# Performance work log

Hardware: AMD Instinct MI355X
Metric: run time of the kernel (lower is better)

The kernel has to match this reference:

```python
import jax, jax.numpy as jnp
import numpy as np

B, T, D, H = 4096, 256, 64, 256


def _uniform(key, shape, bound):
    return jax.random.uniform(key, shape, jnp.float32, -bound, bound)


def setup_inputs() -> dict:
    key = jax.random.key(0)
    ks = jax.random.split(key, 12)
    bnd = 1.0 / np.sqrt(H)
    return {
        "x": jax.random.normal(ks[0], (B, T, D), jnp.float32),
        "h_1": jnp.zeros((B, H), jnp.float32),
        "h_2": jnp.zeros((B, H), jnp.float32),
        # GRUCell 1: input D -> hidden H (PyTorch layout: [3H, in])
        "W_ih1": _uniform(ks[1], (3 * H, D), bnd),
        "W_hh1": _uniform(ks[2], (3 * H, H), bnd),
        "b_ih1": _uniform(ks[3], (3 * H,), bnd),
        "b_hh1": _uniform(ks[4], (3 * H,), bnd),
        # GRUCell 2: input H -> hidden H
        "W_ih2": _uniform(ks[5], (3 * H, H), bnd),
        "W_hh2": _uniform(ks[6], (3 * H, H), bnd),
        "b_ih2": _uniform(ks[7], (3 * H,), bnd),
        "b_hh2": _uniform(ks[8], (3 * H,), bnd),
        # Linear head H -> D
        "W_fc": _uniform(ks[9], (D, H), bnd),
        "b_fc": _uniform(ks[10], (D,), bnd),
    }


def gru_cell(x, h, W_ih, W_hh, b_ih, b_hh):
    # PyTorch GRUCell math: r,z,n gates stacked along first axis of W.
    gi = x @ W_ih.T + b_ih            # [B, 3H]
    gh = h @ W_hh.T + b_hh            # [B, 3H]
    i_r, i_z, i_n = jnp.split(gi, 3, axis=-1)
    h_r, h_z, h_n = jnp.split(gh, 3, axis=-1)
    r = jax.nn.sigmoid(i_r + h_r)
    z = jax.nn.sigmoid(i_z + h_z)
    n = jnp.tanh(i_n + r * h_n)
    return (1.0 - z) * n + z * h


def reference(x, h_1, h_2, W_ih1, W_hh1, b_ih1, b_hh1,
              W_ih2, W_hh2, b_ih2, b_hh2, W_fc, b_fc):
    xs = jnp.swapaxes(x, 0, 1)  # [T, B, D] for scan over time

    def step(carry, x_t):
        h1, h2 = carry
        h1 = gru_cell(x_t, h1, W_ih1, W_hh1, b_ih1, b_hh1)
        h2 = gru_cell(h1, h2, W_ih2, W_hh2, b_ih2, b_hh2)
        y_t = h2 @ W_fc.T + b_fc  # [B, D]
        return (h1, h2), y_t

    (h_1, h_2), ys = jax.lax.scan(step, (h_1, h_2), xs)
    output_seq = jnp.swapaxes(ys, 0, 1)  # [B, T, D]
    return output_seq, h_1, h_2
```

## Files before the change

### kernel.cpp

```cpp
#include <hip/hip_runtime.h>

#define Bn 4096
#define Tn 256
#define Dn 64
#define Hn 256

#define BT  32
#define NTH 512
#define NWG 128
#define LDH 264
#define LDX 72

typedef __attribute__((ext_vector_type(4))) float f32x4;
typedef __attribute__((ext_vector_type(8))) short bf16x8;
typedef __attribute__((ext_vector_type(4))) short s16x4;

#define MFMA16(a,b,c) __builtin_amdgcn_mfma_f32_16x16x32_bf16((a),(b),(c),0,0,0)

#define OFF_WIH1 0
#define OFF_WHH1 49152
#define OFF_WIH2 245760
#define OFF_WHH2 442368
#define OFF_WFC  638976
#define W_TOTAL  655360

__device__ __forceinline__ short f2b(float f){
  union { float fv; unsigned u; } v; v.fv = f;
  unsigned r = v.u + 0x7fffu + ((v.u >> 16) & 1u);
  return (short)(r >> 16);
}
__device__ __forceinline__ float sigm(float x){ return 1.f/(1.f+__expf(-x)); }
__device__ __forceinline__ float tanh_s(float x){ float e=__expf(2.f*x); return 1.f - 2.f/(e+1.f); }

__global__ void prep_weights(const float* __restrict__ Wih1, const float* __restrict__ Whh1,
                             const float* __restrict__ Wih2, const float* __restrict__ Whh2,
                             const float* __restrict__ Wfc, short* __restrict__ wsb){
  for (int i = blockIdx.x*blockDim.x + threadIdx.x; i < W_TOTAL; i += gridDim.x*blockDim.x){
    float v;
    if (i < OFF_WHH1)      v = Wih1[i - OFF_WIH1];
    else if (i < OFF_WIH2) v = Whh1[i - OFF_WHH1];
    else if (i < OFF_WHH2) v = Wih2[i - OFF_WIH2];
    else if (i < OFF_WFC)  v = Whh2[i - OFF_WHH2];
    else                   v = Wfc [i - OFF_WFC];
    wsb[i] = f2b(v);
  }
}

__global__ __launch_bounds__(NTH, 2) void gru_fused(
    const float* __restrict__ x,
    const float* __restrict__ h1_in, const float* __restrict__ h2_in,
    const float* __restrict__ b_ih1, const float* __restrict__ b_hh1,
    const float* __restrict__ b_ih2, const float* __restrict__ b_hh2,
    const float* __restrict__ b_fc,
    const short* __restrict__ wsb,
    float* __restrict__ out)
{
  __shared__ short h1b[BT*LDH];
  __shared__ short h2b[BT*LDH];
  __shared__ short xb [BT*LDX];

  const int tid = (int)threadIdx.x;
  const int w   = tid >> 6;
  const int l   = tid & 63;
  const int q   = l >> 4;
  const int r16 = l & 15;
  const int b0  = (int)blockIdx.x * BT;

  const short* Wih1 = wsb + OFF_WIH1;
  const short* Whh1 = wsb + OFF_WHH1;
  const short* Wih2 = wsb + OFF_WIH2;
  const short* Whh2 = wsb + OFF_WHH2;
  const short* Wfc  = wsb + OFF_WFC;

  float bi1[2][3], bh1v[2][3], bi2[2][3], bh2v[2][3];
#pragma unroll
  for (int c=0;c<2;++c)
#pragma unroll
    for (int g=0;g<3;++g){
      const int col = g*Hn + (2*w+c)*16 + r16;
      bi1 [c][g] = b_ih1[col];  bh1v[c][g] = b_hh1[col];
      bi2 [c][g] = b_ih2[col];  bh2v[c][g] = b_hh2[col];
    }
  const float bfc = b_fc[(w&3)*16 + r16];

  float h1s[2][2][4], h2s[2][2][4];
#pragma unroll
  for (int rt=0;rt<2;++rt)
#pragma unroll
    for (int c=0;c<2;++c)
#pragma unroll
      for (int j=0;j<4;++j){
        const int row = rt*16 + q*4 + j;
        const int col = (2*w+c)*16 + r16;
        const float v1 = h1_in[(size_t)(b0+row)*Hn + col];
        const float v2 = h2_in[(size_t)(b0+row)*Hn + col];
        h1s[rt][c][j] = v1;  h2s[rt][c][j] = v2;
        h1b[row*LDH + col] = f2b(v1);
        h2b[row*LDH + col] = f2b(v2);
      }
  __syncthreads();

  const int xr = tid >> 4;
  const int xd = (tid & 15) * 4;
  const f32x4 z4 = {0.f,0.f,0.f,0.f};

  for (int t=0; t<Tn; ++t){
    {
      const float4 xv = *(const float4*)(x + ((size_t)(b0+xr)*Tn + t)*Dn + xd);
      s16x4 pk; pk.x=f2b(xv.x); pk.y=f2b(xv.y); pk.z=f2b(xv.z); pk.w=f2b(xv.w);
      *(s16x4*)&xb[xr*LDX + xd] = pk;
    }
    __syncthreads();

    f32x4 gi[2][2][3], gh[2][2][3];
#pragma unroll
    for (int rt=0;rt<2;++rt)
#pragma unroll
      for (int c=0;c<2;++c)
#pragma unroll
        for (int g=0;g<3;++g){ gi[rt][c][g]=z4; gh[rt][c][g]=z4; }

#pragma unroll
    for (int k=0;k<2;++k){
      const bf16x8 ax0 = *(const bf16x8*)&xb[(r16   )*LDX + k*32 + q*8];
      const bf16x8 ax1 = *(const bf16x8*)&xb[(16+r16)*LDX + k*32 + q*8];
#pragma unroll
      for (int c=0;c<2;++c)
#pragma unroll
        for (int g=0;g<3;++g){
          const int col = g*Hn + (2*w+c)*16;
          const bf16x8 bx = *(const bf16x8*)&Wih1[(size_t)(col + r16)*Dn + k*32 + q*8];
          gi[0][c][g] = MFMA16(ax0, bx, gi[0][c][g]);
          gi[1][c][g] = MFMA16(ax1, bx, gi[1][c][g]);
        }
    }
    for (int k=0;k<8;++k){
      const bf16x8 a0 = *(const bf16x8*)&h1b[(r16   )*LDH + k*32 + q*8];
      const bf16x8 a1 = *(const bf16x8*)&h1b[(16+r16)*LDH + k*32 + q*8];
#pragma unroll
      for (int c=0;c<2;++c)
#pragma unroll
        for (int g=0;g<3;++g){
          const int col = g*Hn + (2*w+c)*16;
          const bf16x8 bb = *(const bf16x8*)&Whh1[(size_t)(col + r16)*Hn + k*32 + q*8];
          gh[0][c][g] = MFMA16(a0, bb, gh[0][c][g]);
          gh[1][c][g] = MFMA16(a1, bb, gh[1][c][g]);
        }
    }
    __syncthreads();

#pragma unroll
    for (int rt=0;rt<2;++rt)
#pragma unroll
      for (int c=0;c<2;++c){
        const int colb = (2*w+c)*16 + r16;
#pragma unroll
        for (int j=0;j<4;++j){
          const float rr = sigm(gi[rt][c][0][j]+bi1[c][0] + gh[rt][c][0][j]+bh1v[c][0]);
          const float zz = sigm(gi[rt][c][1][j]+bi1[c][1] + gh[rt][c][1][j]+bh1v[c][1]);
          const float nn = tanh_s(gi[rt][c][2][j]+bi1[c][2] + rr*(gh[rt][c][2][j]+bh1v[c][2]));
          const float hv = (1.f-zz)*nn + zz*h1s[rt][c][j];
          h1s[rt][c][j] = hv;
          h1b[(rt*16 + q*4 + j)*LDH + colb] = f2b(hv);
        }
      }
    __syncthreads();

#pragma unroll
    for (int rt=0;rt<2;++rt)
#pragma unroll
      for (int c=0;c<2;++c)
#pragma unroll
        for (int g=0;g<3;++g){ gi[rt][c][g]=z4; gh[rt][c][g]=z4; }

    for (int k=0;k<8;++k){
      const bf16x8 p0 = *(const bf16x8*)&h1b[(r16   )*LDH + k*32 + q*8];
      const bf16x8 p1 = *(const bf16x8*)&h1b[(16+r16)*LDH + k*32 + q*8];
      const bf16x8 s0 = *(const bf16x8*)&h2b[(r16   )*LDH + k*32 + q*8];
      const bf16x8 s1 = *(const bf16x8*)&h2b[(16+r16)*LDH + k*32 + q*8];
#pragma unroll
      for (int c=0;c<2;++c)
#pragma unroll
        for (int g=0;g<3;++g){
          const int col = g*Hn + (2*w+c)*16;
          const bf16x8 wi = *(const bf16x8*)&Wih2[(size_t)(col + r16)*Hn + k*32 + q*8];
          const bf16x8 wh = *(const bf16x8*)&Whh2[(size_t)(col + r16)*Hn + k*32 + q*8];
          gi[0][c][g] = MFMA16(p0, wi, gi[0][c][g]);
          gi[1][c][g] = MFMA16(p1, wi, gi[1][c][g]);
          gh[0][c][g] = MFMA16(s0, wh, gh[0][c][g]);
          gh[1][c][g] = MFMA16(s1, wh, gh[1][c][g]);
        }
    }
    __syncthreads();

#pragma unroll
    for (int rt=0;rt<2;++rt)
#pragma unroll
      for (int c=0;c<2;++c){
        const int colb = (2*w+c)*16 + r16;
#pragma unroll
        for (int j=0;j<4;++j){
          const float rr = sigm(gi[rt][c][0][j]+bi2[c][0] + gh[rt][c][0][j]+bh2v[c][0]);
          const float zz = sigm(gi[rt][c][1][j]+bi2[c][1] + gh[rt][c][1][j]+bh2v[c][1]);
          const float nn = tanh_s(gi[rt][c][2][j]+bi2[c][2] + rr*(gh[rt][c][2][j]+bh2v[c][2]));
          const float hv = (1.f-zz)*nn + zz*h2s[rt][c][j];
          h2s[rt][c][j] = hv;
          h2b[(rt*16 + q*4 + j)*LDH + colb] = f2b(hv);
        }
      }
    __syncthreads();

    {
      const int rt = w >> 2, ct = w & 3;
      f32x4 acc = z4;
      for (int k=0;k<8;++k){
        const bf16x8 a = *(const bf16x8*)&h2b[(rt*16 + r16)*LDH + k*32 + q*8];
        const bf16x8 b = *(const bf16x8*)&Wfc[(size_t)(ct*16 + r16)*Hn + k*32 + q*8];
        acc = MFMA16(a, b, acc);
      }
#pragma unroll
      for (int j=0;j<4;++j){
        out[((size_t)(b0 + rt*16 + q*4 + j)*Tn + t)*Dn + ct*16 + r16] = acc[j] + bfc;
      }
    }
  }

  const size_t offH1 = (size_t)Bn*Tn*Dn;
  const size_t offH2 = offH1 + (size_t)Bn*Hn;
#pragma unroll
  for (int rt=0;rt<2;++rt)
#pragma unroll
    for (int c=0;c<2;++c)
#pragma unroll
      for (int j=0;j<4;++j){
        const int row = b0 + rt*16 + q*4 + j;
        const int col = (2*w+c)*16 + r16;
        out[offH1 + (size_t)row*Hn + col] = h1s[rt][c][j];
        out[offH2 + (size_t)row*Hn + col] = h2s[rt][c][j];
      }
}

extern "C" void kernel_launch(void* const* d_in, const int* in_sizes, int n_in,
                              void* d_out, int out_size, void* d_ws, size_t ws_size,
                              hipStream_t stream) {
  const float* x    = (const float*)d_in[0];
  const float* h1i  = (const float*)d_in[1];
  const float* h2i  = (const float*)d_in[2];
  const float* Wih1 = (const float*)d_in[3];
  const float* Whh1 = (const float*)d_in[4];
  const float* bih1 = (const float*)d_in[5];
  const float* bhh1 = (const float*)d_in[6];
  const float* Wih2 = (const float*)d_in[7];
  const float* Whh2 = (const float*)d_in[8];
  const float* bih2 = (const float*)d_in[9];
  const float* bhh2 = (const float*)d_in[10];
  const float* Wfc  = (const float*)d_in[11];
  const float* bfc  = (const float*)d_in[12];
  short* wsb = (short*)d_ws;
  float* out = (float*)d_out;

  hipLaunchKernelGGL(prep_weights, dim3(512), dim3(256), 0, stream,
                     Wih1, Whh1, Wih2, Whh2, Wfc, wsb);
  hipLaunchKernelGGL(gru_fused, dim3(NWG), dim3(NTH), 0, stream,
                     x, h1i, h2i, bih1, bhh1, bih2, bhh2, bfc, wsb, out);
}
```

Before: 11.57 ms.

## Fragment-tile weights, double-buffer hidden states, load x directly into registers

Weights are re-laid out by the prep kernel into MFMA fragment order, so each lane's 16-byte weight load becomes one fully coalesced contiguous read instead of a strided row gather. The hidden-state LDS buffers are double-buffered (cur/nxt), which removes two of the five barriers per timestep. The x tile is loaded from global straight into register fragments, dropping the LDS staging and its barrier. Inner k loops are fully unrolled, which raises register pressure under the 2-waves-per-SIMD launch bound.

```diff
diff --git a/kernel.cpp b/kernel.cpp
--- a/kernel.cpp
+++ b/kernel.cpp
@@ -9,11 +9,9 @@
 #define NTH 512
 #define NWG 128
 #define LDH 264
-#define LDX 72
 
 typedef __attribute__((ext_vector_type(4))) float f32x4;
 typedef __attribute__((ext_vector_type(8))) short bf16x8;
-typedef __attribute__((ext_vector_type(4))) short s16x4;
 
 #define MFMA16(a,b,c) __builtin_amdgcn_mfma_f32_16x16x32_bf16((a),(b),(c),0,0,0)
 
@@ -36,13 +34,17 @@
                              const float* __restrict__ Wih2, const float* __restrict__ Whh2,
                              const float* __restrict__ Wfc, short* __restrict__ wsb){
   for (int i = blockIdx.x*blockDim.x + threadIdx.x; i < W_TOTAL; i += gridDim.x*blockDim.x){
-    float v;
-    if (i < OFF_WHH1)      v = Wih1[i - OFF_WIH1];
-    else if (i < OFF_WIH2) v = Whh1[i - OFF_WHH1];
-    else if (i < OFF_WHH2) v = Wih2[i - OFF_WIH2];
-    else if (i < OFF_WFC)  v = Whh2[i - OFF_WHH2];
-    else                   v = Wfc [i - OFF_WFC];
-    wsb[i] = f2b(v);
+    const float* src; int local, K, s;
+    if (i < OFF_WHH1)      { src = Wih1; local = i - OFF_WIH1; K = 64;  s = 1; }
+    else if (i < OFF_WIH2) { src = Whh1; local = i - OFF_WHH1; K = 256; s = 3; }
+    else if (i < OFF_WHH2) { src = Wih2; local = i - OFF_WIH2; K = 256; s = 3; }
+    else if (i < OFF_WFC)  { src = Whh2; local = i - OFF_WHH2; K = 256; s = 3; }
+    else                   { src = Wfc;  local = i - OFF_WFC;  K = 256; s = 3; }
+    const int blk = local >> 9, e9 = local & 511;
+    const int q = e9 >> 7, r16 = (e9 >> 3) & 15, e = e9 & 7;
+    const int cb = blk >> s, k = blk & ((1 << s) - 1);
+    const int row = cb*16 + r16, col = k*32 + q*8 + e;
+    wsb[i] = f2b(src[row*K + col]);
   }
 }
 
@@ -55,9 +57,8 @@
     const short* __restrict__ wsb,
     float* __restrict__ out)
 {
-  __shared__ short h1b[BT*LDH];
-  __shared__ short h2b[BT*LDH];
-  __shared__ short xb [BT*LDX];
+  __shared__ short H1[2][BT*LDH];
+  __shared__ short H2[2][BT*LDH];
 
   const int tid = (int)threadIdx.x;
   const int w   = tid >> 6;
@@ -66,11 +67,11 @@
   const int r16 = l & 15;
   const int b0  = (int)blockIdx.x * BT;
 
-  const short* Wih1 = wsb + OFF_WIH1;
-  const short* Whh1 = wsb + OFF_WHH1;
-  const short* Wih2 = wsb + OFF_WIH2;
-  const short* Whh2 = wsb + OFF_WHH2;
-  const short* Wfc  = wsb + OFF_WFC;
+  const short* __restrict__ Wih1f = wsb + OFF_WIH1;
+  const short* __restrict__ Whh1f = wsb + OFF_WHH1;
+  const short* __restrict__ Wih2f = wsb + OFF_WIH2;
+  const short* __restrict__ Whh2f = wsb + OFF_WHH2;
+  const short* __restrict__ Wfcf  = wsb + OFF_WFC;
 
   float bi1[2][3], bh1v[2][3], bi2[2][3], bh2v[2][3];
 #pragma unroll
@@ -95,22 +96,29 @@
         const float v1 = h1_in[(size_t)(b0+row)*Hn + col];
         const float v2 = h2_in[(size_t)(b0+row)*Hn + col];
         h1s[rt][c][j] = v1;  h2s[rt][c][j] = v2;
-        h1b[row*LDH + col] = f2b(v1);
-        h2b[row*LDH + col] = f2b(v2);
+        H1[0][row*LDH + col] = f2b(v1);
+        H2[0][row*LDH + col] = f2b(v2);
       }
   __syncthreads();
 
-  const int xr = tid >> 4;
-  const int xd = (tid & 15) * 4;
   const f32x4 z4 = {0.f,0.f,0.f,0.f};
 
   for (int t=0; t<Tn; ++t){
-    {
-      const float4 xv = *(const float4*)(x + ((size_t)(b0+xr)*Tn + t)*Dn + xd);
-      s16x4 pk; pk.x=f2b(xv.x); pk.y=f2b(xv.y); pk.z=f2b(xv.z); pk.w=f2b(xv.w);
-      *(s16x4*)&xb[xr*LDX + xd] = pk;
-    }
-    __syncthreads();
+    const int cur = t & 1, nxt = cur ^ 1;
+
+    bf16x8 ax[2][2];
+#pragma unroll
+    for (int rt=0;rt<2;++rt)
+#pragma unroll
+      for (int k=0;k<2;++k){
+        const float* xp = x + ((size_t)(b0 + rt*16 + r16)*Tn + t)*Dn + k*32 + q*8;
+        const float4 v0 = *(const float4*)xp;
+        const float4 v1 = *(const float4*)(xp+4);
+        bf16x8 a;
+        a[0]=f2b(v0.x); a[1]=f2b(v0.y); a[2]=f2b(v0.z); a[3]=f2b(v0.w);
+        a[4]=f2b(v1.x); a[5]=f2b(v1.y); a[6]=f2b(v1.z); a[7]=f2b(v1.w);
+        ax[rt][k] = a;
+      }
 
     f32x4 gi[2][2][3], gh[2][2][3];
 #pragma unroll
@@ -121,33 +129,31 @@
         for (int g=0;g<3;++g){ gi[rt][c][g]=z4; gh[rt][c][g]=z4; }
 
 #pragma unroll
-    for (int k=0;k<2;++k){
-      const bf16x8 ax0 = *(const bf16x8*)&xb[(r16   )*LDX + k*32 + q*8];
-      const bf16x8 ax1 = *(const bf16x8*)&xb[(16+r16)*LDX + k*32 + q*8];
+    for (int k=0;k<2;++k)
 #pragma unroll
       for (int c=0;c<2;++c)
 #pragma unroll
         for (int g=0;g<3;++g){
-          const int col = g*Hn + (2*w+c)*16;
-          const bf16x8 bx = *(const bf16x8*)&Wih1[(size_t)(col + r16)*Dn + k*32 + q*8];
-          gi[0][c][g] = MFMA16(ax0, bx, gi[0][c][g]);
-          gi[1][c][g] = MFMA16(ax1, bx, gi[1][c][g]);
-        }
-    }
+          const int cb = g*16 + 2*w + c;
+          const bf16x8 bx = *(const bf16x8*)&Wih1f[(((cb<<1)+k)<<9) + (l<<3)];
+          gi[0][c][g] = MFMA16(ax[0][k], bx, gi[0][c][g]);
+          gi[1][c][g] = MFMA16(ax[1][k], bx, gi[1][c][g]);
+        }
+
+#pragma unroll
     for (int k=0;k<8;++k){
-      const bf16x8 a0 = *(const bf16x8*)&h1b[(r16   )*LDH + k*32 + q*8];
-      const bf16x8 a1 = *(const bf16x8*)&h1b[(16+r16)*LDH + k*32 + q*8];
+      const bf16x8 a0 = *(const bf16x8*)&H1[cur][(r16   )*LDH + k*32 + q*8];
+      const bf16x8 a1 = *(const bf16x8*)&H1[cur][(16+r16)*LDH + k*32 + q*8];
 #pragma unroll
       for (int c=0;c<2;++c)
 #pragma unroll
         for (int g=0;g<3;++g){
-          const int col = g*Hn + (2*w+c)*16;
-          const bf16x8 bb = *(const bf16x8*)&Whh1[(size_t)(col + r16)*Hn + k*32 + q*8];
+          const int cb = g*16 + 2*w + c;
+          const bf16x8 bb = *(const bf16x8*)&Whh1f[(((cb<<3)+k)<<9) + (l<<3)];
           gh[0][c][g] = MFMA16(a0, bb, gh[0][c][g]);
           gh[1][c][g] = MFMA16(a1, bb, gh[1][c][g]);
         }
     }
-    __syncthreads();
 
 #pragma unroll
     for (int rt=0;rt<2;++rt)
@@ -161,7 +167,7 @@
           const float nn = tanh_s(gi[rt][c][2][j]+bi1[c][2] + rr*(gh[rt][c][2][j]+bh1v[c][2]));
           const float hv = (1.f-zz)*nn + zz*h1s[rt][c][j];
           h1s[rt][c][j] = hv;
-          h1b[(rt*16 + q*4 + j)*LDH + colb] = f2b(hv);
+          H1[nxt][(rt*16 + q*4 + j)*LDH + colb] = f2b(hv);
         }
       }
     __syncthreads();
@@ -173,25 +179,25 @@
 #pragma unroll
         for (int g=0;g<3;++g){ gi[rt][c][g]=z4; gh[rt][c][g]=z4; }
 
+#pragma unroll
     for (int k=0;k<8;++k){
-      const bf16x8 p0 = *(const bf16x8*)&h1b[(r16   )*LDH + k*32 + q*8];
-      const bf16x8 p1 = *(const bf16x8*)&h1b[(16+r16)*LDH + k*32 + q*8];
-      const bf16x8 s0 = *(const bf16x8*)&h2b[(r16   )*LDH + k*32 + q*8];
-      const bf16x8 s1 = *(const bf16x8*)&h2b[(16+r16)*LDH + k*32 + q*8];
+      const bf16x8 p0 = *(const bf16x8*)&H1[nxt][(r16   )*LDH + k*32 + q*8];
+      const bf16x8 p1 = *(const bf16x8*)&H1[nxt][(16+r16)*LDH + k*32 + q*8];
+      const bf16x8 s0 = *(const bf16x8*)&H2[cur][(r16   )*LDH + k*32 + q*8];
+      const bf16x8 s1 = *(const bf16x8*)&H2[cur][(16+r16)*LDH + k*32 + q*8];
 #pragma unroll
       for (int c=0;c<2;++c)
 #pragma unroll
         for (int g=0;g<3;++g){
-          const int col = g*Hn + (2*w+c)*16;
-          const bf16x8 wi = *(const bf16x8*)&Wih2[(size_t)(col + r16)*Hn + k*32 + q*8];
-          const bf16x8 wh = *(const bf16x8*)&Whh2[(size_t)(col + r16)*Hn + k*32 + q*8];
+          const int cb = g*16 + 2*w + c;
+          const bf16x8 wi = *(const bf16x8*)&Wih2f[(((cb<<3)+k)<<9) + (l<<3)];
+          const bf16x8 wh = *(const bf16x8*)&Whh2f[(((cb<<3)+k)<<9) + (l<<3)];
           gi[0][c][g] = MFMA16(p0, wi, gi[0][c][g]);
           gi[1][c][g] = MFMA16(p1, wi, gi[1][c][g]);
           gh[0][c][g] = MFMA16(s0, wh, gh[0][c][g]);
           gh[1][c][g] = MFMA16(s1, wh, gh[1][c][g]);
         }
     }
-    __syncthreads();
 
 #pragma unroll
     for (int rt=0;rt<2;++rt)
@@ -205,22 +211,23 @@
           const float nn = tanh_s(gi[rt][c][2][j]+bi2[c][2] + rr*(gh[rt][c][2][j]+bh2v[c][2]));
           const float hv = (1.f-zz)*nn + zz*h2s[rt][c][j];
           h2s[rt][c][j] = hv;
-          h2b[(rt*16 + q*4 + j)*LDH + colb] = f2b(hv);
+          H2[nxt][(rt*16 + q*4 + j)*LDH + colb] = f2b(hv);
         }
       }
     __syncthreads();
 
     {
-      const int rt = w >> 2, ct = w & 3;
+      const int rtw = w >> 2, ct = w & 3;
       f32x4 acc = z4;
+#pragma unroll
       for (int k=0;k<8;++k){
-        const bf16x8 a = *(const bf16x8*)&h2b[(rt*16 + r16)*LDH + k*32 + q*8];
-        const bf16x8 b = *(const bf16x8*)&Wfc[(size_t)(ct*16 + r16)*Hn + k*32 + q*8];
+        const bf16x8 a = *(const bf16x8*)&H2[nxt][(rtw*16 + r16)*LDH + k*32 + q*8];
+        const bf16x8 b = *(const bf16x8*)&Wfcf[(((ct<<3)+k)<<9) + (l<<3)];
         acc = MFMA16(a, b, acc);
       }
 #pragma unroll
       for (int j=0;j<4;++j){
-        out[((size_t)(b0 + rt*16 + q*4 + j)*Tn + t)*Dn + ct*16 + r16] = acc[j] + bfc;
+        out[((size_t)(b0 + rtw*16 + q*4 + j)*Tn + t)*Dn + ct*16 + r16] = acc[j] + bfc;
       }
     }
   }
```

New measurement: 14.45 ms. 1.25x slower.
